# Optimization experiments

Measured on AMD Instinct MI355X. Metric: run time of the kernel, lower is better.

Reference implementation:

```python
import jax, jax.numpy as jnp
import numpy as np

# Graph/block sizes: batch=1024 output nodes, fanouts [15,10,5] outer->inner layer
N_SRC0 = 1081344
N_DST = (67584, 6144, 1024)
FANOUT = (15, 10, 5)
DIMS = ((128, 256), (256, 256), (256, 47))  # (in, out) per layer


def setup_inputs() -> dict:
    key = jax.random.key(0)
    ks = jax.random.split(key, 16)
    inp = {
        "x": jax.random.normal(ks[0], (N_SRC0, DIMS[0][0]), dtype=jnp.float32),
        "neigh0": jax.random.randint(ks[1], (N_DST[0], FANOUT[0]), 0, N_SRC0, dtype=jnp.int32),
        "neigh1": jax.random.randint(ks[2], (N_DST[1], FANOUT[1]), 0, N_DST[0], dtype=jnp.int32),
        "neigh2": jax.random.randint(ks[3], (N_DST[2], FANOUT[2]), 0, N_DST[1], dtype=jnp.int32),
    }
    for l, (din, dout) in enumerate(DIMS):
        s = 1.0 / np.sqrt(din)
        inp[f"Wself{l}"] = jax.random.normal(ks[4 + 3 * l], (din, dout), dtype=jnp.float32) * s
        inp[f"Wneigh{l}"] = jax.random.normal(ks[5 + 3 * l], (din, dout), dtype=jnp.float32) * s
        inp[f"b{l}"] = jnp.zeros((dout,), dtype=jnp.float32)
    return inp


def _sage_layer(h, neigh, Wself, Wneigh, b):
    # DGL SAGEConv('mean') on a bipartite block: dst nodes are the prefix of src nodes.
    h_neigh = jnp.mean(h[neigh], axis=1)          # [n_dst, d_in] gather + mean over fanout
    h_dst = h[: neigh.shape[0]]                    # [n_dst, d_in]
    return h_dst @ Wself + h_neigh @ Wneigh + b


def reference(x, neigh0, neigh1, neigh2,
              Wself0, Wneigh0, b0, Wself1, Wneigh1, b1, Wself2, Wneigh2, b2):
    # dropout is identity in eval mode; activation = relu on all but last layer
    h = jax.nn.relu(_sage_layer(x, neigh0, Wself0, Wneigh0, b0))
    h = jax.nn.relu(_sage_layer(h, neigh1, Wself1, Wneigh1, b1))
    return _sage_layer(h, neigh2, Wself2, Wneigh2, b2)  # [1024, 47]
```

## Files before the change

kernel.cpp:

```cpp
#include <hip/hip_runtime.h>

using bf16x8 = __attribute__((ext_vector_type(8))) short;
using f32x4  = __attribute__((ext_vector_type(4))) float;

__device__ __forceinline__ short f2bf(float x) {
    union { float f; unsigned u; } v; v.f = x;
    unsigned r = v.u + 0x7fffu + ((v.u >> 16) & 1u);
    return (short)(r >> 16);
}
__device__ __forceinline__ float bf2f(short h) {
    union { unsigned u; float f; } v; v.u = ((unsigned)(unsigned short)h) << 16;
    return v.f;
}

template<int DIN>
__device__ __forceinline__ void pack_one(int blk, const float* __restrict__ Wself,
                                         const float* __restrict__ Wneigh,
                                         short* __restrict__ Wp, int l)
{
    const int ks  = blk >> 4, nt = blk & 15;
    const int col = nt * 16 + (l & 15);
    const int k0  = ks * 32 + (l >> 4) * 8;

    bf16x8 hi;
    #pragma unroll
    for (int e = 0; e < 8; ++e) {
        int k = k0 + e;
        float w = (k < DIN) ? Wself[k * 256 + col] : Wneigh[(k - DIN) * 256 + col];
        hi[e] = f2bf(w);
    }
    *reinterpret_cast<bf16x8*>(Wp + (size_t)blk * 512 + l * 8) = hi;
}

__global__ __launch_bounds__(64)
void pack_w_all(const float* __restrict__ Ws0, const float* __restrict__ Wn0,
                short* __restrict__ Wp0,
                const float* __restrict__ Ws1, const float* __restrict__ Wn1,
                short* __restrict__ Wp1)
{
    const int b = blockIdx.x, l = threadIdx.x;
    if (b < 128) pack_one<128>(b, Ws0, Wn0, Wp0, l);
    else         pack_one<256>(b - 128, Ws1, Wn1, Wp1, l);
}

template<int DIN, int F, int RB, int NTW, bool IN_BF16, bool OUT_BF16, bool RELU>
__global__ __launch_bounds__(256)
void sage_mfma(const void* __restrict__ h_in_v,
               const int*   __restrict__ neigh,
               const short* __restrict__ Wp,
               const float* __restrict__ bias,
               void* __restrict__ h_out_v)
{
    constexpr int KS    = DIN / 16;
    constexpr int KSH   = DIN / 32;
    constexpr int LROW  = DIN + 4;
    constexpr int WROWS = RB / 16;
    constexpr int WCOLS = 16 / NTW;
    static_assert(WROWS * WCOLS == 4, "4 waves");
    constexpr float invF = 1.0f / F;

    __shared__ float An[RB][LROW];
    __shared__ int   nb[RB * F];

    const int  tid = threadIdx.x;
    const int  w   = tid >> 6, l = tid & 63;
    const int  lr  = l & 15, lk = l >> 4;
    const long r0  = (long)blockIdx.x * RB;
    const int  wrow = (w % WROWS) * 16;
    const int  nt0  = (w / WROWS) * NTW;

    for (int p = tid; p < RB * F; p += 256)
        nb[p] = neigh[r0 * F + p];
    __syncthreads();

    if constexpr (!IN_BF16) {
        constexpr int QD = DIN / 4;
        const float* hin = (const float*)h_in_v;
        for (int p = tid; p < RB * QD; p += 256) {
            int m = p / QD, q = p - m * QD;
            float4 a = make_float4(0.f, 0.f, 0.f, 0.f);
            #pragma unroll
            for (int n = 0; n < F; ++n) {
                long idx = nb[m * F + n];
                float4 v = reinterpret_cast<const float4*>(hin + idx * DIN)[q];
                a.x += v.x; a.y += v.y; a.z += v.z; a.w += v.w;
            }
            a.x *= invF; a.y *= invF; a.z *= invF; a.w *= invF;
            *reinterpret_cast<float4*>(&An[m][q * 4]) = a;
        }
    } else {
        constexpr int NQ = DIN / 8;
        const short* hin = (const short*)h_in_v;
        for (int p = tid; p < RB * NQ; p += 256) {
            int m = p / NQ, c = p - m * NQ;
            float a[8] = {0.f,0.f,0.f,0.f,0.f,0.f,0.f,0.f};
            #pragma unroll
            for (int n = 0; n < F; ++n) {
                long idx = nb[m * F + n];
                bf16x8 v = *reinterpret_cast<const bf16x8*>(hin + idx * DIN + c * 8);
                #pragma unroll
                for (int e = 0; e < 8; ++e) a[e] += bf2f(v[e]);
            }
            #pragma unroll
            for (int e = 0; e < 8; ++e) a[e] *= invF;
            *reinterpret_cast<float4*>(&An[m][c * 8])     = make_float4(a[0],a[1],a[2],a[3]);
            *reinterpret_cast<float4*>(&An[m][c * 8 + 4]) = make_float4(a[4],a[5],a[6],a[7]);
        }
    }
    __syncthreads();

    const float* selfrowF = (const float*)h_in_v + (r0 + wrow + lr) * DIN;
    const short* selfrowB = (const short*)h_in_v + (r0 + wrow + lr) * DIN;
    const float* neighrow = &An[wrow + lr][0];

    f32x4 acc[NTW];
    #pragma unroll
    for (int j = 0; j < NTW; ++j) acc[j] = f32x4{0.f, 0.f, 0.f, 0.f};

    for (int ks = 0; ks < KS; ++ks) {
        bf16x8 ah, al;
        bool self_exact = false;
        if (ks < KSH) {
            if constexpr (IN_BF16) {
                ah = *reinterpret_cast<const bf16x8*>(selfrowB + ks * 32 + lk * 8);
                self_exact = true;
            } else {
                const int k0 = ks * 32 + lk * 8;
                float4 t0 = *reinterpret_cast<const float4*>(selfrowF + k0);
                float4 t1 = *reinterpret_cast<const float4*>(selfrowF + k0 + 4);
                float v[8] = {t0.x, t0.y, t0.z, t0.w, t1.x, t1.y, t1.z, t1.w};
                #pragma unroll
                for (int e = 0; e < 8; ++e) {
                    short h = f2bf(v[e]);
                    ah[e] = h;
                    al[e] = f2bf(v[e] - bf2f(h));
                }
            }
        } else {
            const int k0 = (ks - KSH) * 32 + lk * 8;
            float4 t0 = *reinterpret_cast<const float4*>(neighrow + k0);
            float4 t1 = *reinterpret_cast<const float4*>(neighrow + k0 + 4);
            float v[8] = {t0.x, t0.y, t0.z, t0.w, t1.x, t1.y, t1.z, t1.w};
            #pragma unroll
            for (int e = 0; e < 8; ++e) {
                short h = f2bf(v[e]);
                ah[e] = h;
                al[e] = f2bf(v[e] - bf2f(h));
            }
        }

        const bf16x8* wp = reinterpret_cast<const bf16x8*>(Wp) +
                           (size_t)(ks * 16 + nt0) * 64;
        #pragma unroll
        for (int j = 0; j < NTW; ++j) {
            bf16x8 bh = wp[j * 64 + l];
            acc[j] = __builtin_amdgcn_mfma_f32_16x16x32_bf16(ah, bh, acc[j], 0, 0, 0);
            if (!self_exact)
                acc[j] = __builtin_amdgcn_mfma_f32_16x16x32_bf16(al, bh, acc[j], 0, 0, 0);
        }
    }

    #pragma unroll
    for (int j = 0; j < NTW; ++j) {
        const int col = (nt0 + j) * 16 + lr;
        const float b = bias[col];
        #pragma unroll
        for (int r = 0; r < 4; ++r) {
            const long row = r0 + wrow + lk * 4 + r;
            float val = acc[j][r] + b;
            if (RELU) val = fmaxf(val, 0.f);
            if constexpr (OUT_BF16)
                ((short*)h_out_v)[row * 256 + col] = f2bf(val);
            else
                ((float*)h_out_v)[row * 256 + col] = val;
        }
    }
}

__global__ __launch_bounds__(64)
void sage_out(const float* __restrict__ h_in,
              const int*   __restrict__ neigh,
              const float* __restrict__ Wself,
              const float* __restrict__ Wneigh,
              const float* __restrict__ bias,
              float* __restrict__ out)
{
    __shared__ float hs[256], hn[256];
    __shared__ int   nb[5];
    const int r = blockIdx.x, tid = threadIdx.x;

    if (tid < 5) nb[tid] = neigh[r * 5 + tid];
    __syncthreads();

    for (int k = tid; k < 256; k += 64) {
        hs[k] = h_in[(long)r * 256 + k];
        float a = 0.f;
        #pragma unroll
        for (int n = 0; n < 5; ++n) a += h_in[(long)nb[n] * 256 + k];
        hn[k] = a * 0.2f;
    }
    __syncthreads();

    if (tid < 47) {
        float acc = bias[tid];
        for (int k = 0; k < 256; ++k)
            acc += hs[k] * Wself[k * 47 + tid] + hn[k] * Wneigh[k * 47 + tid];
        out[r * 47 + tid] = acc;
    }
}

extern "C" void kernel_launch(void* const* d_in, const int* in_sizes, int n_in,
                              void* d_out, int out_size, void* d_ws, size_t ws_size,
                              hipStream_t stream)
{
    const float* x   = (const float*)d_in[0];
    const int*   n0  = (const int*)  d_in[1];
    const int*   n1  = (const int*)  d_in[2];
    const int*   n2  = (const int*)  d_in[3];
    const float* Ws0 = (const float*)d_in[4];
    const float* Wn0 = (const float*)d_in[5];
    const float* b0  = (const float*)d_in[6];
    const float* Ws1 = (const float*)d_in[7];
    const float* Wn1 = (const float*)d_in[8];
    const float* b1  = (const float*)d_in[9];
    const float* Ws2 = (const float*)d_in[10];
    const float* Wn2 = (const float*)d_in[11];
    const float* b2  = (const float*)d_in[12];
    float* out = (float*)d_out;

    short* h1  = (short*)d_ws;
    float* h2  = (float*)(h1 + (size_t)67584 * 256);
    short* Wp0 = (short*)(h2 + (size_t)6144 * 256);
    short* Wp1 = Wp0 + (size_t)128 * 512;

    pack_w_all<<<384, 64, 0, stream>>>(Ws0, Wn0, Wp0, Ws1, Wn1, Wp1);

    sage_mfma<128, 15, 32, 8, false, true,  true><<<67584 / 32, 256, 0, stream>>>(x,  n0, Wp0, b0, h1);
    sage_mfma<256, 10, 16, 4,  true,  false, true><<<6144 / 16,  256, 0, stream>>>(h1, n1, Wp1, b1, h2);
    sage_out<<<1024, 64, 0, stream>>>(h2, n2, Ws2, Wn2, b2, out);
}
```

Baseline: 151.1 us.

## Compute only layer-0 rows that layer 1 actually references

Adds three small kernels: one clears a mask, one marks every h1 row that layer 1 reads (the dst prefix plus all neigh1 targets), and one compacts the marked rows into a list with an atomic counter. The layer-0 MFMA kernel gains a COMPACT mode that reads row ids from this list, gathers neighbours and self rows through it, and scatters its outputs back to the original row positions. Blocks past the live count exit early. With random neighbour indices a large share of h1 rows is never read, so this skips that gather and GEMM work. The cost is three extra launches, scattered self-row reads and output writes, and an ordering that depends on the atomics.

After: 140.6 us. 6.9% less time.

```diff
diff --git a/kernel.cpp b/kernel.cpp
--- a/kernel.cpp
+++ b/kernel.cpp
@@ -11,6 +11,30 @@
 __device__ __forceinline__ float bf2f(short h) {
     union { unsigned u; float f; } v; v.u = ((unsigned)(unsigned short)h) << 16;
     return v.f;
+}
+
+__global__ __launch_bounds__(256)
+void k_clear(unsigned* __restrict__ mask, unsigned* __restrict__ count, int n)
+{
+    int i = blockIdx.x * 256 + threadIdx.x;
+    if (i < n) mask[i] = 0;
+    if (i == 0) *count = 0;
+}
+
+__global__ __launch_bounds__(256)
+void k_mark(const int* __restrict__ neigh1, unsigned* __restrict__ mask)
+{
+    int j = blockIdx.x * 256 + threadIdx.x;
+    if (j < 6144) mask[j] = 1;
+    else if (j < 67584) mask[neigh1[j - 6144]] = 1;
+}
+
+__global__ __launch_bounds__(256)
+void k_compact(const unsigned* __restrict__ mask, unsigned* __restrict__ list,
+               unsigned* __restrict__ count, int n)
+{
+    int i = blockIdx.x * 256 + threadIdx.x;
+    if (i < n && mask[i]) list[atomicAdd(count, 1u)] = i;
 }
 
 template<int DIN>
@@ -43,13 +67,15 @@
     else         pack_one<256>(b - 128, Ws1, Wn1, Wp1, l);
 }
 
-template<int DIN, int F, int RB, int NTW, bool IN_BF16, bool OUT_BF16, bool RELU>
+template<int DIN, int F, int RB, int NTW, bool COMPACT, bool IN_BF16, bool OUT_BF16, bool RELU>
 __global__ __launch_bounds__(256)
 void sage_mfma(const void* __restrict__ h_in_v,
                const int*   __restrict__ neigh,
                const short* __restrict__ Wp,
                const float* __restrict__ bias,
-               void* __restrict__ h_out_v)
+               void* __restrict__ h_out_v,
+               const unsigned* __restrict__ list,
+               const unsigned* __restrict__ count)
 {
     constexpr int KS    = DIN / 16;
     constexpr int KSH   = DIN / 32;
@@ -59,8 +85,10 @@
     static_assert(WROWS * WCOLS == 4, "4 waves");
     constexpr float invF = 1.0f / F;
 
-    __shared__ float An[RB][LROW];
-    __shared__ int   nb[RB * F];
+    __shared__ float    An[RB][LROW];
+    __shared__ int      nb[RB * F];
+    __shared__ unsigned rids[RB];
+    __shared__ unsigned scnt;
 
     const int  tid = threadIdx.x;
     const int  w   = tid >> 6, l = tid & 63;
@@ -69,8 +97,19 @@
     const int  wrow = (w % WROWS) * 16;
     const int  nt0  = (w / WROWS) * NTW;
 
-    for (int p = tid; p < RB * F; p += 256)
-        nb[p] = neigh[r0 * F + p];
+    if constexpr (COMPACT) {
+        if (tid == 0) scnt = *count;
+        __syncthreads();
+        if (r0 >= (long)scnt) return;
+        for (int p = tid; p < RB; p += 256)
+            rids[p] = (r0 + p < (long)scnt) ? list[r0 + p] : list[0];
+        __syncthreads();
+        for (int p = tid; p < RB * F; p += 256)
+            nb[p] = neigh[(long)rids[p / F] * F + (p % F)];
+    } else {
+        for (int p = tid; p < RB * F; p += 256)
+            nb[p] = neigh[r0 * F + p];
+    }
     __syncthreads();
 
     if constexpr (!IN_BF16) {
@@ -109,8 +148,9 @@
     }
     __syncthreads();
 
-    const float* selfrowF = (const float*)h_in_v + (r0 + wrow + lr) * DIN;
-    const short* selfrowB = (const short*)h_in_v + (r0 + wrow + lr) * DIN;
+    const long selfrid = COMPACT ? (long)rids[wrow + lr] : (r0 + wrow + lr);
+    const float* selfrowF = (const float*)h_in_v + selfrid * DIN;
+    const short* selfrowB = (const short*)h_in_v + selfrid * DIN;
     const float* neighrow = &An[wrow + lr][0];
 
     f32x4 acc[NTW];
@@ -166,7 +206,9 @@
         const float b = bias[col];
         #pragma unroll
         for (int r = 0; r < 4; ++r) {
-            const long row = r0 + wrow + lk * 4 + r;
+            const int slot = wrow + lk * 4 + r;
+            if (COMPACT && (r0 + slot >= (long)scnt)) continue;
+            const long row = COMPACT ? (long)rids[slot] : (r0 + slot);
             float val = acc[j][r] + b;
             if (RELU) val = fmaxf(val, 0.f);
             if constexpr (OUT_BF16)
@@ -228,14 +270,25 @@
     const float* b2  = (const float*)d_in[12];
     float* out = (float*)d_out;
 
-    short* h1  = (short*)d_ws;
-    float* h2  = (float*)(h1 + (size_t)67584 * 256);
-    short* Wp0 = (short*)(h2 + (size_t)6144 * 256);
-    short* Wp1 = Wp0 + (size_t)128 * 512;
+    short*    h1   = (short*)d_ws;
+    float*    h2   = (float*)(h1 + (size_t)67584 * 256);
+    short*    Wp0  = (short*)(h2 + (size_t)6144 * 256);
+    short*    Wp1  = Wp0 + (size_t)128 * 512;
+    unsigned* mask = (unsigned*)(Wp1 + (size_t)256 * 512);
+    unsigned* list = mask + 67584;
+    unsigned* cnt  = list + 67584;
+
+    constexpr int M0 = 67584;
+
+    k_clear  <<<(M0 + 255) / 256, 256, 0, stream>>>(mask, cnt, M0);
+    k_mark   <<<(M0 + 255) / 256, 256, 0, stream>>>(n1, mask);
+    k_compact<<<(M0 + 255) / 256, 256, 0, stream>>>(mask, list, cnt, M0);
 
     pack_w_all<<<384, 64, 0, stream>>>(Ws0, Wn0, Wp0, Ws1, Wn1, Wp1);
 
-    sage_mfma<128, 15, 32, 8, false, true,  true><<<67584 / 32, 256, 0, stream>>>(x,  n0, Wp0, b0, h1);
-    sage_mfma<256, 10, 16, 4,  true,  false, true><<<6144 / 16,  256, 0, stream>>>(h1, n1, Wp1, b1, h2);
+    sage_mfma<128, 15, 32, 8, true,  false, true,  true>
+        <<<M0 / 32, 256, 0, stream>>>(x,  n0, Wp0, b0, h1, list, cnt);
+    sage_mfma<256, 10, 16, 4, false, true,  false, true>
+        <<<6144 / 16, 256, 0, stream>>>(h1, n1, Wp1, b1, h2, nullptr, nullptr);
     sage_out<<<1024, 64, 0, stream>>>(h2, n2, Ws2, Wn2, b2, out);
 }
```

## Skip layer-0 rows never read by layer 1 using a needed-row mask

Applied to the files above, without the earlier changes.

A prep kernel builds a per-row mask over layer-0 outputs. It marks every row referenced by neigh1 plus the first 6144 self rows, and it also packs the weights as before. The layer-0 kernel then skips the neighbour gather and the output stores for unmarked rows, which avoids the large random reads of x for rows whose results are never consumed. The final small layer's dot product is also split into four independent accumulators to give more instruction-level parallelism. This adds a memset and scattered mask writes, and the MFMA work for skipped rows is still performed.

Result: faster. 130.9 us (-13.4%).

```diff
diff --git a/kernel.cpp b/kernel.cpp
--- a/kernel.cpp
+++ b/kernel.cpp
@@ -32,24 +32,36 @@
     *reinterpret_cast<bf16x8*>(Wp + (size_t)blk * 512 + l * 8) = hi;
 }
 
-__global__ __launch_bounds__(64)
-void pack_w_all(const float* __restrict__ Ws0, const float* __restrict__ Wn0,
-                short* __restrict__ Wp0,
-                const float* __restrict__ Ws1, const float* __restrict__ Wn1,
-                short* __restrict__ Wp1)
-{
-    const int b = blockIdx.x, l = threadIdx.x;
-    if (b < 128) pack_one<128>(b, Ws0, Wn0, Wp0, l);
-    else         pack_one<256>(b - 128, Ws1, Wn1, Wp1, l);
-}
-
-template<int DIN, int F, int RB, int NTW, bool IN_BF16, bool OUT_BF16, bool RELU>
+__global__ __launch_bounds__(256)
+void k_prep(const int* __restrict__ neigh1, unsigned* __restrict__ mask,
+            const float* __restrict__ Ws0, const float* __restrict__ Wn0,
+            short* __restrict__ Wp0,
+            const float* __restrict__ Ws1, const float* __restrict__ Wn1,
+            short* __restrict__ Wp1)
+{
+    const int b = blockIdx.x, tid = threadIdx.x;
+    if (b < 240) {
+        int j = b * 256 + tid;
+        mask[neigh1[j]] = 1u;
+    } else if (b < 264) {
+        int i = (b - 240) * 256 + tid;
+        mask[i] = 1u;
+    } else {
+        int unit = (b - 264) * 4 + (tid >> 6);
+        int l = tid & 63;
+        if (unit < 128) pack_one<128>(unit, Ws0, Wn0, Wp0, l);
+        else            pack_one<256>(unit - 128, Ws1, Wn1, Wp1, l);
+    }
+}
+
+template<int DIN, int F, int RB, int NTW, bool MASKED, bool IN_BF16, bool OUT_BF16, bool RELU>
 __global__ __launch_bounds__(256)
 void sage_mfma(const void* __restrict__ h_in_v,
                const int*   __restrict__ neigh,
                const short* __restrict__ Wp,
                const float* __restrict__ bias,
-               void* __restrict__ h_out_v)
+               void* __restrict__ h_out_v,
+               const unsigned* __restrict__ mask)
 {
     constexpr int KS    = DIN / 16;
     constexpr int KSH   = DIN / 32;
@@ -59,8 +71,9 @@
     static_assert(WROWS * WCOLS == 4, "4 waves");
     constexpr float invF = 1.0f / F;
 
-    __shared__ float An[RB][LROW];
-    __shared__ int   nb[RB * F];
+    __shared__ float    An[RB][LROW];
+    __shared__ int      nb[RB * F];
+    __shared__ unsigned need[RB];
 
     const int  tid = threadIdx.x;
     const int  w   = tid >> 6, l = tid & 63;
@@ -71,6 +84,10 @@
 
     for (int p = tid; p < RB * F; p += 256)
         nb[p] = neigh[r0 * F + p];
+    if constexpr (MASKED) {
+        for (int p = tid; p < RB; p += 256)
+            need[p] = mask[r0 + p];
+    }
     __syncthreads();
 
     if constexpr (!IN_BF16) {
@@ -78,6 +95,7 @@
         const float* hin = (const float*)h_in_v;
         for (int p = tid; p < RB * QD; p += 256) {
             int m = p / QD, q = p - m * QD;
+            if (MASKED && !need[m]) continue;
             float4 a = make_float4(0.f, 0.f, 0.f, 0.f);
             #pragma unroll
             for (int n = 0; n < F; ++n) {
@@ -93,6 +111,7 @@
         const short* hin = (const short*)h_in_v;
         for (int p = tid; p < RB * NQ; p += 256) {
             int m = p / NQ, c = p - m * NQ;
+            if (MASKED && !need[m]) continue;
             float a[8] = {0.f,0.f,0.f,0.f,0.f,0.f,0.f,0.f};
             #pragma unroll
             for (int n = 0; n < F; ++n) {
@@ -166,7 +185,9 @@
         const float b = bias[col];
         #pragma unroll
         for (int r = 0; r < 4; ++r) {
-            const long row = r0 + wrow + lk * 4 + r;
+            const int slot = wrow + lk * 4 + r;
+            if (MASKED && !need[slot]) continue;
+            const long row = r0 + slot;
             float val = acc[j][r] + b;
             if (RELU) val = fmaxf(val, 0.f);
             if constexpr (OUT_BF16)
@@ -202,10 +223,15 @@
     __syncthreads();
 
     if (tid < 47) {
-        float acc = bias[tid];
-        for (int k = 0; k < 256; ++k)
-            acc += hs[k] * Wself[k * 47 + tid] + hn[k] * Wneigh[k * 47 + tid];
-        out[r * 47 + tid] = acc;
+        float a0 = 0.f, a1 = 0.f, a2 = 0.f, a3 = 0.f;
+        #pragma unroll 4
+        for (int k = 0; k < 256; k += 4) {
+            a0 += hs[k    ] * Wself[(k    ) * 47 + tid] + hn[k    ] * Wneigh[(k    ) * 47 + tid];
+            a1 += hs[k + 1] * Wself[(k + 1) * 47 + tid] + hn[k + 1] * Wneigh[(k + 1) * 47 + tid];
+            a2 += hs[k + 2] * Wself[(k + 2) * 47 + tid] + hn[k + 2] * Wneigh[(k + 2) * 47 + tid];
+            a3 += hs[k + 3] * Wself[(k + 3) * 47 + tid] + hn[k + 3] * Wneigh[(k + 3) * 47 + tid];
+        }
+        out[r * 47 + tid] = bias[tid] + ((a0 + a1) + (a2 + a3));
     }
 }
 
@@ -228,14 +254,23 @@
     const float* b2  = (const float*)d_in[12];
     float* out = (float*)d_out;
 
-    short* h1  = (short*)d_ws;
-    float* h2  = (float*)(h1 + (size_t)67584 * 256);
-    short* Wp0 = (short*)(h2 + (size_t)6144 * 256);
-    short* Wp1 = Wp0 + (size_t)128 * 512;
-
-    pack_w_all<<<384, 64, 0, stream>>>(Ws0, Wn0, Wp0, Ws1, Wn1, Wp1);
-
-    sage_mfma<128, 15, 32, 8, false, true,  true><<<67584 / 32, 256, 0, stream>>>(x,  n0, Wp0, b0, h1);
-    sage_mfma<256, 10, 16, 4,  true,  false, true><<<6144 / 16,  256, 0, stream>>>(h1, n1, Wp1, b1, h2);
+    short*    h1   = (short*)d_ws;
+    float*    h2   = (float*)(h1 + (size_t)67584 * 256);
+    short*    Wp0  = (short*)(h2 + (size_t)6144 * 256);
+    short*    Wp1  = Wp0 + (size_t)128 * 512;
+    unsigned* mask = (unsigned*)(Wp1 + (size_t)256 * 512);
+
+    constexpr int M0 = 67584;
+
+    hipMemsetAsync(mask, 0, (size_t)M0 * sizeof(unsigned), stream);
+
+    k_prep<<<360, 256, 0, stream>>>(n1, mask, Ws0, Wn0, Wp0, Ws1, Wn1, Wp1);
+
+    sage_mfma<128, 15, 32, 8, true,  false, true,  true>
+        <<<M0 / 32, 256, 0, stream>>>(x,  n0, Wp0, b0, h1, mask);
+
+    sage_mfma<256, 10, 16, 4, false, true,  false, true>
+        <<<6144 / 16, 256, 0, stream>>>(h1, n1, Wp1, b1, h2, nullptr);
+
     sage_out<<<1024, 64, 0, stream>>>(h2, n2, Ws2, Wn2, b2, out);
 }
```
